# Kernel tuning notes

Hardware: AMD Instinct MI355X
Metric: run time of the kernel (lower is better)

Reference implementation:

```python
import jax, jax.numpy as jnp
import numpy as np

DIM = 256
NUM_HEADS = 8


def setup_inputs() -> dict:
    key = jax.random.key(0)
    ks = jax.random.split(key, 5)
    B, V, C, H, W = 4, 6, DIM, 64, 64
    x = jax.random.normal(ks[0], (B, V, C, H, W), dtype=jnp.float32)
    # 1x1 conv weights (out_channels, in_channels), bias=False
    s = 1.0 / np.sqrt(C)
    Wq = jax.random.normal(ks[1], (C, C), dtype=jnp.float32) * s
    Wk = jax.random.normal(ks[2], (C, C), dtype=jnp.float32) * s
    Wv = jax.random.normal(ks[3], (C, C), dtype=jnp.float32) * s
    Wo = jax.random.normal(ks[4], (C, C), dtype=jnp.float32) * s
    return {"x": x, "Wq": Wq, "Wk": Wk, "Wv": Wv, "Wo": Wo}


def reference(x, Wq, Wk, Wv, Wo):
    B, V, C, H, W = x.shape
    h = NUM_HEADS
    dh = C // h
    scale = dh ** (-0.5)

    def proj(Wm):
        # 1x1 conv == per-pixel channel matmul; -> [B, h, V, HW, dh]
        t = jnp.einsum('bvchw,oc->bvohw', x, Wm)
        t = t.reshape(B, V, h, dh, H * W)
        return t.transpose(0, 2, 1, 4, 3)  # b h v w d (w = flattened HW)

    Q = proj(Wq)
    K = proj(Wk)
    Vv = proj(Wv)

    Qloc = Q.mean(axis=2)  # average query over views: [B, h, HW, dh]
    scores = jnp.einsum('bhwd,bhvwd->bhwv', Qloc, K) * scale  # [B, h, HW, V]
    attn = jax.nn.softmax(scores, axis=-1)
    out = jnp.einsum('bhwv,bhvwd->bhwd', attn, Vv)  # [B, h, HW, dh]
    out = out.transpose(0, 1, 3, 2).reshape(B, C, H, W)
    return jnp.einsum('bchw,oc->bohw', out, Wo)  # out_proj 1x1 conv
```

## Files before the change

### kernel.cpp

```cpp
#include <hip/hip_runtime.h>
#include <hip/hip_bf16.h>


typedef __bf16 bf16x8 __attribute__((ext_vector_type(8)));
typedef float f32x4 __attribute__((ext_vector_type(4)));

#define HW 4096
#define C_DIM 256
#define NV 6
#define NB 4

__global__ __launch_bounds__(256) void convert_weights_kernel(
    const float* __restrict__ Wq, const float* __restrict__ Wk,
    const float* __restrict__ Wv, const float* __restrict__ Wo,
    __hip_bfloat16* __restrict__ out)
{
    const float* srcs[4] = {Wq, Wk, Wv, Wo};
    const int m = blockIdx.y;
    const int i = blockIdx.x * 256 + threadIdx.x;
    out[m * 65536 + i] = __float2bfloat16(srcs[m][i]);
}

__global__ __launch_bounds__(256) void transpose_mean_kernel(
    const float* __restrict__ x,
    __hip_bfloat16* __restrict__ xt,
    __hip_bfloat16* __restrict__ xbar)
{
    __shared__ float tile[64][65];
    const int w0 = blockIdx.x * 64;
    const int c0 = blockIdx.y * 64;
    const int b  = blockIdx.z;
    const int t  = threadIdx.x;
    const int li = t & 63;
    const int qi = t >> 6;
    float acc[16];
#pragma unroll
    for (int i = 0; i < 16; ++i) acc[i] = 0.f;

    for (int v = 0; v < NV; ++v) {
        const float* src = x + (((size_t)b * NV + v) * C_DIM + c0) * HW + w0;
#pragma unroll
        for (int i = 0; i < 16; ++i) {
            const int c = qi + 4 * i;
            tile[li][c] = src[(size_t)c * HW + li];
        }
        __syncthreads();
        __hip_bfloat16* dst = xt + (((size_t)b * NV + v) * HW + w0) * C_DIM + c0;
#pragma unroll
        for (int i = 0; i < 16; ++i) {
            const int w = qi + 4 * i;
            const float val = tile[w][li];
            acc[i] += val;
            dst[(size_t)w * C_DIM + li] = __float2bfloat16(val);
        }
        __syncthreads();
    }
    __hip_bfloat16* dbar = xbar + ((size_t)b * HW + w0) * C_DIM + c0;
#pragma unroll
    for (int i = 0; i < 16; ++i) {
        const int w = qi + 4 * i;
        dbar[(size_t)w * C_DIM + li] = __float2bfloat16(acc[i] * (1.f / 6.f));
    }
}

__global__ __launch_bounds__(512) void mega_kernel(
    const __hip_bfloat16* __restrict__ xt,
    const __hip_bfloat16* __restrict__ xbar,
    const __hip_bfloat16* __restrict__ Wq,
    const __hip_bfloat16* __restrict__ Wk,
    const __hip_bfloat16* __restrict__ Wv,
    const __hip_bfloat16* __restrict__ Wo,
    float* __restrict__ out)
{
    __shared__ __align__(16) __hip_bfloat16 Abuf[2][8192];
    __shared__ __align__(16) float T2[256][36];
    const size_t SL = (size_t)HW * C_DIM;
    const int w0 = blockIdx.x * 32;
    const int b  = blockIdx.y;
    const int t  = threadIdx.x, wv = t >> 6, l = t & 63;
    const int kb_l = l >> 4, rl = l & 15, lq = l >> 4;
    const int pr = t >> 1;
    const int px = pr & 31, h = pr >> 5, sub = t & 1;
    const int c0 = h * 32 + sub * 16;

    f32x4 acc[2][2];
    auto zacc = [&]() {
#pragma unroll
        for (int i = 0; i < 2; ++i)
#pragma unroll
            for (int j = 0; j < 2; ++j) {
                acc[i][j][0] = 0.f; acc[i][j][1] = 0.f;
                acc[i][j][2] = 0.f; acc[i][j][3] = 0.f;
            }
    };

    auto stageA = [&](int buf, const __hip_bfloat16* src) {
#pragma unroll
        for (int c2 = 0; c2 < 2; ++c2) {
            const int ch = wv * 2 + c2;
            const int kb = ch * 2 + (l >> 5);
            const __hip_bfloat16* g = src + (size_t)(w0 + (l & 31)) * 256 + kb * 8;
            __builtin_amdgcn_global_load_lds(
                (const __attribute__((address_space(1))) void*)g,
                (__attribute__((address_space(3))) void*)(&Abuf[buf][ch * 512]),
                16, 0, 0);
        }
    };

    auto gemmStream = [&](int buf, const __hip_bfloat16* W) {
        const __hip_bfloat16* wb = W + (size_t)(wv * 32 + rl) * 256 + kb_l * 8;
        bf16x8 bq[4][2];
#pragma unroll
        for (int p = 0; p < 3; ++p)
#pragma unroll
            for (int j = 0; j < 2; ++j)
                bq[p][j] = *(const bf16x8*)(wb + p * 32 + j * 4096);
#pragma unroll
        for (int kt = 0; kt < 8; ++kt) {
            if (kt + 3 < 8) {
#pragma unroll
                for (int j = 0; j < 2; ++j)
                    bq[(kt + 3) & 3][j] = *(const bf16x8*)(wb + (kt + 3) * 32 + j * 4096);
            }
            bf16x8 af[2];
#pragma unroll
            for (int i = 0; i < 2; ++i)
                af[i] = *(const bf16x8*)&Abuf[buf][(kt * 4 + kb_l) * 256 + (i * 16 + rl) * 8];
#pragma unroll
            for (int i = 0; i < 2; ++i)
#pragma unroll
                for (int j = 0; j < 2; ++j)
                    acc[i][j] = __builtin_amdgcn_mfma_f32_16x16x32_bf16(af[i], bq[kt & 3][j], acc[i][j], 0, 0, 0);
        }
    };

    auto writeT2 = [&]() {
#pragma unroll
        for (int i = 0; i < 2; ++i)
#pragma unroll
            for (int j = 0; j < 2; ++j)
                *(f32x4*)&T2[wv * 32 + j * 16 + rl][i * 16 + lq * 4] = acc[i][j];
    };

    stageA(0, xbar + (size_t)b * SL);
    __syncthreads();
    zacc();
    gemmStream(0, Wq);
    stageA(1, xt + (size_t)(b * NV) * SL);
    writeT2();
    __syncthreads();

    const float scale = 0.17677669529663687f;
    bf16x8 qbf[2];
#pragma unroll
    for (int i = 0; i < 2; ++i)
#pragma unroll
        for (int j = 0; j < 8; ++j)
            qbf[i][j] = (__bf16)(T2[c0 + i * 8 + j][px] * scale);

    float m = -1e30f, den = 0.f;
    float o[16];
#pragma unroll
    for (int cc = 0; cc < 16; ++cc) o[cc] = 0.f;

    for (int v = 0; v < NV; ++v) {
        const int buf = (v + 1) & 1;
        __syncthreads();
        if (v < NV - 1) stageA(buf ^ 1, xt + (size_t)(b * NV + v + 1) * SL);
        zacc();
        gemmStream(buf, Wk);
        writeT2();
        __syncthreads();

        float s = 0.f;
#pragma unroll
        for (int i = 0; i < 2; ++i)
#pragma unroll
            for (int j = 0; j < 8; ++j)
                s += (float)qbf[i][j] * T2[c0 + i * 8 + j][px];
        s += __shfl_xor(s, 1);
        const float mn = fmaxf(m, s);
        const float f  = __expf(m - mn);
        const float e  = __expf(s - mn);
        den = den * f + e;
        m = mn;
#pragma unroll
        for (int cc = 0; cc < 16; ++cc) o[cc] *= f;
        __syncthreads();

        zacc();
        gemmStream(buf, Wv);
        writeT2();
        __syncthreads();
#pragma unroll
        for (int cc = 0; cc < 16; ++cc) o[cc] += e * T2[c0 + cc][px];
    }

    const float inv = 1.f / den;
#pragma unroll
    for (int k2 = 0; k2 < 2; ++k2) {
        bf16x8 ov;
#pragma unroll
        for (int k = 0; k < 8; ++k) ov[k] = (__bf16)(o[k2 * 8 + k] * inv);
        const int kb = (c0 >> 3) + k2;
        *(bf16x8*)&Abuf[0][kb * 256 + px * 8] = ov;
    }
    __syncthreads();
    zacc();
    gemmStream(0, Wo);

    float* op = out + (size_t)b * C_DIM * HW;
#pragma unroll
    for (int i = 0; i < 2; ++i)
#pragma unroll
        for (int j = 0; j < 2; ++j) {
            const int col = wv * 32 + j * 16 + rl;
            *(f32x4*)(op + (size_t)col * HW + w0 + i * 16 + lq * 4) = acc[i][j];
        }
}

extern "C" void kernel_launch(void* const* d_in, const int* in_sizes, int n_in,
                              void* d_out, int out_size, void* d_ws, size_t ws_size,
                              hipStream_t stream)
{
    const float* x  = (const float*)d_in[0];
    const float* Wq = (const float*)d_in[1];
    const float* Wk = (const float*)d_in[2];
    const float* Wv = (const float*)d_in[3];
    const float* Wo = (const float*)d_in[4];
    (void)in_sizes; (void)n_in; (void)out_size; (void)ws_size;

    char* ws = (char*)d_ws;
    const size_t MB = 1024ull * 1024ull;
    const size_t SL = (size_t)HW * C_DIM;

    __hip_bfloat16* Wbf  = (__hip_bfloat16*)(ws);
    __hip_bfloat16* xt   = (__hip_bfloat16*)(ws + 1 * MB);
    __hip_bfloat16* xbar = (__hip_bfloat16*)(ws + 49 * MB);

    const __hip_bfloat16* WqB = Wbf;
    const __hip_bfloat16* WkB = Wbf + 65536;
    const __hip_bfloat16* WvB = Wbf + 131072;
    const __hip_bfloat16* WoB = Wbf + 196608;

    convert_weights_kernel<<<dim3(256, 4), 256, 0, stream>>>(Wq, Wk, Wv, Wo, Wbf);
    transpose_mean_kernel<<<dim3(HW / 64, C_DIM / 64, NB), 256, 0, stream>>>(x, xt, xbar);
    mega_kernel<<<dim3(HW / 32, NB), 512, 0, stream>>>(xt, xbar, WqB, WkB, WvB, WoB, (float*)d_out);
}
```

Measured before the change: 114.5 us.

## Fuse K/V projection GEMMs and run attention softmax directly on MFMA accumulators

Merges the separate K and V projection passes into one GEMM loop that shares the A fragments. The online softmax now runs on the MFMA accumulator registers, with head-wise reductions done by lane shuffles, so the T2 shared-memory round trip and most per-view barriers go away. The staging buffer gains padding to reduce LDS bank conflicts. The cost is higher register pressure (K, V and output accumulators live together), and the weight-prefetch software pipeline is dropped.

```diff
diff --git a/kernel.cpp b/kernel.cpp
--- a/kernel.cpp
+++ b/kernel.cpp
@@ -3,6 +3,7 @@
 
 
 typedef __bf16 bf16x8 __attribute__((ext_vector_type(8)));
+typedef __bf16 bf16x4 __attribute__((ext_vector_type(4)));
 typedef float f32x4 __attribute__((ext_vector_type(4)));
 
 #define HW 4096
@@ -72,142 +73,152 @@
     const __hip_bfloat16* __restrict__ Wo,
     float* __restrict__ out)
 {
-    __shared__ __align__(16) __hip_bfloat16 Abuf[2][8192];
-    __shared__ __align__(16) float T2[256][36];
+    __shared__ __align__(16) __hip_bfloat16 Abuf[2][8320];
     const size_t SL = (size_t)HW * C_DIM;
     const int w0 = blockIdx.x * 32;
     const int b  = blockIdx.y;
     const int t  = threadIdx.x, wv = t >> 6, l = t & 63;
-    const int kb_l = l >> 4, rl = l & 15, lq = l >> 4;
-    const int pr = t >> 1;
-    const int px = pr & 31, h = pr >> 5, sub = t & 1;
-    const int c0 = h * 32 + sub * 16;
-
-    f32x4 acc[2][2];
-    auto zacc = [&]() {
-#pragma unroll
-        for (int i = 0; i < 2; ++i)
-#pragma unroll
-            for (int j = 0; j < 2; ++j) {
-                acc[i][j][0] = 0.f; acc[i][j][1] = 0.f;
-                acc[i][j][2] = 0.f; acc[i][j][3] = 0.f;
-            }
-    };
+    const int g = l >> 4, rl = l & 15;
 
     auto stageA = [&](int buf, const __hip_bfloat16* src) {
 #pragma unroll
         for (int c2 = 0; c2 < 2; ++c2) {
             const int ch = wv * 2 + c2;
             const int kb = ch * 2 + (l >> 5);
-            const __hip_bfloat16* g = src + (size_t)(w0 + (l & 31)) * 256 + kb * 8;
+            const __hip_bfloat16* gp = src + (size_t)(w0 + (l & 31)) * 256 + kb * 8;
             __builtin_amdgcn_global_load_lds(
-                (const __attribute__((address_space(1))) void*)g,
-                (__attribute__((address_space(3))) void*)(&Abuf[buf][ch * 512]),
+                (const __attribute__((address_space(1))) void*)gp,
+                (__attribute__((address_space(3))) void*)(&Abuf[buf][ch * 520]),
                 16, 0, 0);
         }
     };
 
-    auto gemmStream = [&](int buf, const __hip_bfloat16* W) {
-        const __hip_bfloat16* wb = W + (size_t)(wv * 32 + rl) * 256 + kb_l * 8;
-        bf16x8 bq[4][2];
-#pragma unroll
-        for (int p = 0; p < 3; ++p)
-#pragma unroll
-            for (int j = 0; j < 2; ++j)
-                bq[p][j] = *(const bf16x8*)(wb + p * 32 + j * 4096);
+    auto ldA = [&](int buf, int kt, int i) -> bf16x8 {
+        const int kb = kt * 4 + g;
+        return *(const bf16x8*)&Abuf[buf][(kb >> 1) * 520 + (kb & 1) * 256 + (i * 16 + rl) * 8];
+    };
+    auto ldB = [&](const __hip_bfloat16* W, int j, int kt) -> bf16x8 {
+        return *(const bf16x8*)(W + (size_t)(wv * 32 + j * 16 + rl) * 256 + kt * 32 + g * 8);
+    };
+
+    f32x4 Kacc[2][2], Vacc[2][2], oacc[2][2];
+
+    auto gemm1 = [&](int buf, const __hip_bfloat16* W) {
+#pragma unroll
+        for (int i = 0; i < 2; ++i)
+#pragma unroll
+            for (int j = 0; j < 2; ++j) {
+                Kacc[i][j][0] = 0.f; Kacc[i][j][1] = 0.f;
+                Kacc[i][j][2] = 0.f; Kacc[i][j][3] = 0.f;
+            }
 #pragma unroll
         for (int kt = 0; kt < 8; ++kt) {
-            if (kt + 3 < 8) {
-#pragma unroll
-                for (int j = 0; j < 2; ++j)
-                    bq[(kt + 3) & 3][j] = *(const bf16x8*)(wb + (kt + 3) * 32 + j * 4096);
-            }
-            bf16x8 af[2];
-#pragma unroll
-            for (int i = 0; i < 2; ++i)
-                af[i] = *(const bf16x8*)&Abuf[buf][(kt * 4 + kb_l) * 256 + (i * 16 + rl) * 8];
-#pragma unroll
-            for (int i = 0; i < 2; ++i)
-#pragma unroll
-                for (int j = 0; j < 2; ++j)
-                    acc[i][j] = __builtin_amdgcn_mfma_f32_16x16x32_bf16(af[i], bq[kt & 3][j], acc[i][j], 0, 0, 0);
-        }
-    };
-
-    auto writeT2 = [&]() {
+            bf16x8 b0 = ldB(W, 0, kt), b1 = ldB(W, 1, kt);
+            bf16x8 a0 = ldA(buf, kt, 0), a1 = ldA(buf, kt, 1);
+            Kacc[0][0] = __builtin_amdgcn_mfma_f32_16x16x32_bf16(a0, b0, Kacc[0][0], 0, 0, 0);
+            Kacc[0][1] = __builtin_amdgcn_mfma_f32_16x16x32_bf16(a0, b1, Kacc[0][1], 0, 0, 0);
+            Kacc[1][0] = __builtin_amdgcn_mfma_f32_16x16x32_bf16(a1, b0, Kacc[1][0], 0, 0, 0);
+            Kacc[1][1] = __builtin_amdgcn_mfma_f32_16x16x32_bf16(a1, b1, Kacc[1][1], 0, 0, 0);
+        }
+    };
+
+    auto gemmKV = [&](int buf) {
 #pragma unroll
         for (int i = 0; i < 2; ++i)
 #pragma unroll
-            for (int j = 0; j < 2; ++j)
-                *(f32x4*)&T2[wv * 32 + j * 16 + rl][i * 16 + lq * 4] = acc[i][j];
+            for (int j = 0; j < 2; ++j) {
+#pragma unroll
+                for (int r = 0; r < 4; ++r) { Kacc[i][j][r] = 0.f; Vacc[i][j][r] = 0.f; }
+            }
+#pragma unroll
+        for (int kt = 0; kt < 8; ++kt) {
+            bf16x8 bk0 = ldB(Wk, 0, kt), bk1 = ldB(Wk, 1, kt);
+            bf16x8 bv0 = ldB(Wv, 0, kt), bv1 = ldB(Wv, 1, kt);
+            bf16x8 a0 = ldA(buf, kt, 0), a1 = ldA(buf, kt, 1);
+            Kacc[0][0] = __builtin_amdgcn_mfma_f32_16x16x32_bf16(a0, bk0, Kacc[0][0], 0, 0, 0);
+            Vacc[0][0] = __builtin_amdgcn_mfma_f32_16x16x32_bf16(a0, bv0, Vacc[0][0], 0, 0, 0);
+            Kacc[0][1] = __builtin_amdgcn_mfma_f32_16x16x32_bf16(a0, bk1, Kacc[0][1], 0, 0, 0);
+            Vacc[0][1] = __builtin_amdgcn_mfma_f32_16x16x32_bf16(a0, bv1, Vacc[0][1], 0, 0, 0);
+            Kacc[1][0] = __builtin_amdgcn_mfma_f32_16x16x32_bf16(a1, bk0, Kacc[1][0], 0, 0, 0);
+            Vacc[1][0] = __builtin_amdgcn_mfma_f32_16x16x32_bf16(a1, bv0, Vacc[1][0], 0, 0, 0);
+            Kacc[1][1] = __builtin_amdgcn_mfma_f32_16x16x32_bf16(a1, bk1, Kacc[1][1], 0, 0, 0);
+            Vacc[1][1] = __builtin_amdgcn_mfma_f32_16x16x32_bf16(a1, bv1, Vacc[1][1], 0, 0, 0);
+        }
     };
 
     stageA(0, xbar + (size_t)b * SL);
     __syncthreads();
-    zacc();
-    gemmStream(0, Wq);
+    gemm1(0, Wq);
     stageA(1, xt + (size_t)(b * NV) * SL);
-    writeT2();
+
+    const float scale = 0.17677669529663687f;
+    bf16x4 qb[2][2];
+#pragma unroll
+    for (int i = 0; i < 2; ++i)
+#pragma unroll
+        for (int j = 0; j < 2; ++j)
+#pragma unroll
+            for (int r = 0; r < 4; ++r)
+                qb[i][j][r] = (__bf16)(Kacc[i][j][r] * scale);
+
+    float m[2][4], den[2][4];
+#pragma unroll
+    for (int i = 0; i < 2; ++i)
+#pragma unroll
+        for (int r = 0; r < 4; ++r) { m[i][r] = -1e30f; den[i][r] = 0.f; }
+#pragma unroll
+    for (int i = 0; i < 2; ++i)
+#pragma unroll
+        for (int j = 0; j < 2; ++j) {
+            oacc[i][j][0] = 0.f; oacc[i][j][1] = 0.f;
+            oacc[i][j][2] = 0.f; oacc[i][j][3] = 0.f;
+        }
     __syncthreads();
-
-    const float scale = 0.17677669529663687f;
-    bf16x8 qbf[2];
-#pragma unroll
-    for (int i = 0; i < 2; ++i)
-#pragma unroll
-        for (int j = 0; j < 8; ++j)
-            qbf[i][j] = (__bf16)(T2[c0 + i * 8 + j][px] * scale);
-
-    float m = -1e30f, den = 0.f;
-    float o[16];
-#pragma unroll
-    for (int cc = 0; cc < 16; ++cc) o[cc] = 0.f;
 
     for (int v = 0; v < NV; ++v) {
         const int buf = (v + 1) & 1;
+        if (v < NV - 1) stageA(buf ^ 1, xt + (size_t)(b * NV + v + 1) * SL);
+        gemmKV(buf);
+
+#pragma unroll
+        for (int i = 0; i < 2; ++i)
+#pragma unroll
+            for (int r = 0; r < 4; ++r) {
+                float s = (float)qb[i][0][r] * Kacc[i][0][r]
+                        + (float)qb[i][1][r] * Kacc[i][1][r];
+                s += __shfl_xor(s, 1);
+                s += __shfl_xor(s, 2);
+                s += __shfl_xor(s, 4);
+                s += __shfl_xor(s, 8);
+                const float mn = fmaxf(m[i][r], s);
+                const float f  = __expf(m[i][r] - mn);
+                const float e  = __expf(s - mn);
+                den[i][r] = den[i][r] * f + e;
+                m[i][r]   = mn;
+#pragma unroll
+                for (int j = 0; j < 2; ++j) {
+                    oacc[i][j][r] = oacc[i][j][r] * f + e * Vacc[i][j][r];
+                }
+            }
         __syncthreads();
-        if (v < NV - 1) stageA(buf ^ 1, xt + (size_t)(b * NV + v + 1) * SL);
-        zacc();
-        gemmStream(buf, Wk);
-        writeT2();
-        __syncthreads();
-
-        float s = 0.f;
-#pragma unroll
-        for (int i = 0; i < 2; ++i)
-#pragma unroll
-            for (int j = 0; j < 8; ++j)
-                s += (float)qbf[i][j] * T2[c0 + i * 8 + j][px];
-        s += __shfl_xor(s, 1);
-        const float mn = fmaxf(m, s);
-        const float f  = __expf(m - mn);
-        const float e  = __expf(s - mn);
-        den = den * f + e;
-        m = mn;
-#pragma unroll
-        for (int cc = 0; cc < 16; ++cc) o[cc] *= f;
-        __syncthreads();
-
-        zacc();
-        gemmStream(buf, Wv);
-        writeT2();
-        __syncthreads();
-#pragma unroll
-        for (int cc = 0; cc < 16; ++cc) o[cc] += e * T2[c0 + cc][px];
     }
 
-    const float inv = 1.f / den;
-#pragma unroll
-    for (int k2 = 0; k2 < 2; ++k2) {
-        bf16x8 ov;
-#pragma unroll
-        for (int k = 0; k < 8; ++k) ov[k] = (__bf16)(o[k2 * 8 + k] * inv);
-        const int kb = (c0 >> 3) + k2;
-        *(bf16x8*)&Abuf[0][kb * 256 + px * 8] = ov;
-    }
+#pragma unroll
+    for (int i = 0; i < 2; ++i)
+#pragma unroll
+        for (int r = 0; r < 4; ++r) {
+            const float inv = 1.f / den[i][r];
+            const int row = i * 16 + g * 4 + r;
+#pragma unroll
+            for (int j = 0; j < 2; ++j) {
+                const int c  = wv * 32 + j * 16 + rl;
+                const int kb = c >> 3;
+                Abuf[0][(kb >> 1) * 520 + (kb & 1) * 256 + row * 8 + (c & 7)] =
+                    __float2bfloat16(oacc[i][j][r] * inv);
+            }
+        }
     __syncthreads();
-    zacc();
-    gemmStream(0, Wo);
+    gemm1(0, Wo);
 
     float* op = out + (size_t)b * C_DIM * HW;
 #pragma unroll
@@ -215,7 +226,7 @@
 #pragma unroll
         for (int j = 0; j < 2; ++j) {
             const int col = wv * 32 + j * 16 + rl;
-            *(f32x4*)(op + (size_t)col * HW + w0 + i * 16 + lq * 4) = acc[i][j];
+            *(f32x4*)(op + (size_t)col * HW + w0 + i * 16 + g * 4) = Kacc[i][j];
         }
 }
 
```

Result: faster. 107.7 us (-6.0%).
